# Kernel optimization log

Hardware: AMD Instinct MI355X
Metric: run time of the kernel (lower is better)

The kernel has to match this reference:

```python
import jax, jax.numpy as jnp
import numpy as np

B = 1
L_IMG, L_TMP, L_TXT = 1024, 1024, 256
D, H, HD, MLP = 1024, 16, 64, 4096
L = L_TXT + L_IMG + L_TMP
EPS = 1e-6
ATTN_SCALE = float(1.0 / np.sqrt(HD))


def setup_inputs() -> dict:
    key = jax.random.key(0)
    ks = jax.random.split(key, 12)
    s = 0.02  # keep activations stable
    return {
        'img': jax.random.normal(ks[0], (B, L_IMG, D), jnp.float32),
        'temporal': jax.random.normal(ks[1], (B, L_TMP, D), jnp.float32),
        'txt': jax.random.normal(ks[2], (B, L_TXT, D), jnp.float32),
        'vec': jax.random.normal(ks[3], (B, D), jnp.float32),
        'pe': jax.random.normal(ks[4], (B, 1, L, HD // 2, 2, 2), jnp.float32),
        'mod_w': jax.random.normal(ks[5], (3, D, 6 * D), jnp.float32) * s,
        'mod_b': jnp.zeros((3, 6 * D), jnp.float32),
        'qkv_w': jax.random.normal(ks[6], (3, D, 3 * D), jnp.float32) * s,
        'q_scale': jnp.ones((3, HD), jnp.float32),
        'k_scale': jnp.ones((3, HD), jnp.float32),
        'proj_w': jax.random.normal(ks[7], (3, D, D), jnp.float32) * s,
        'proj_b': jnp.zeros((3, D), jnp.float32),
        'mlp_w1': jax.random.normal(ks[8], (3, D, MLP), jnp.float32) * s,
        'mlp_b1': jnp.zeros((3, MLP), jnp.float32),
        'mlp_w2': jax.random.normal(ks[9], (3, MLP, D), jnp.float32) * s,
        'mlp_b2': jnp.zeros((3, D), jnp.float32),
    }


def _ln(x):
    # LayerNorm, elementwise_affine=False, eps=1e-6
    m = jnp.mean(x, axis=-1, keepdims=True)
    v = jnp.mean((x - m) ** 2, axis=-1, keepdims=True)
    return (x - m) * jax.lax.rsqrt(v + EPS)


def _rms(x, scale):
    # flux QKNorm RMSNorm with learnable per-head-dim scale
    return x * jax.lax.rsqrt(jnp.mean(x * x, axis=-1, keepdims=True) + EPS) * scale


def _rope(x, pe):
    # x: (B,H,L,HD), pe: (B,1,L,HD//2,2,2)
    xr = x.reshape(*x.shape[:-1], -1, 1, 2)
    out = pe[..., 0] * xr[..., 0] + pe[..., 1] * xr[..., 1]  # (B,H,L,HD//2,2)
    return out.reshape(x.shape)


def _forward(img, temporal, txt, vec, pe, mod_w, mod_b, qkv_w, q_scale, k_scale,
             proj_w, proj_b, mlp_w1, mlp_b1, mlp_w2, mlp_b2):
    sv = jax.nn.silu(vec)  # (B,D)

    def mods(i):
        m = (sv @ mod_w[i] + mod_b[i])[:, None, :]  # (B,1,6D)
        return jnp.split(m, 6, axis=-1)  # shift1, scale1, gate1, shift2, scale2, gate2

    def qkv_stream(x, i, shift1, scale1):
        xm = (1.0 + scale1) * _ln(x) + shift1
        qkv = (xm @ qkv_w[i]).reshape(x.shape[0], x.shape[1], 3, H, HD)
        q, k, v = jnp.moveaxis(qkv, 2, 0)  # each (B,Ls,H,HD)
        q = jnp.swapaxes(q, 1, 2)
        k = jnp.swapaxes(k, 1, 2)
        v = jnp.swapaxes(v, 1, 2)  # (B,H,Ls,HD)
        return _rms(q, q_scale[i]), _rms(k, k_scale[i]), v

    i_sh1, i_sc1, i_g1, i_sh2, i_sc2, i_g2 = mods(0)
    t_sh1, t_sc1, t_g1, t_sh2, t_sc2, t_g2 = mods(1)
    x_sh1, x_sc1, x_g1, x_sh2, x_sc2, x_g2 = mods(2)

    img_q, img_k, img_v = qkv_stream(img, 0, i_sh1, i_sc1)
    tmp_q, tmp_k, tmp_v = qkv_stream(temporal, 1, t_sh1, t_sc1)
    txt_q, txt_k, txt_v = qkv_stream(txt, 2, x_sh1, x_sc1)

    q = jnp.concatenate((txt_q, img_q, tmp_q), axis=2)
    k = jnp.concatenate((txt_k, img_k, tmp_k), axis=2)
    # NOTE: faithful to source bug: v concat uses temporal_q, not temporal_v
    v = jnp.concatenate((txt_v, img_v, tmp_q), axis=2)

    q = _rope(q, pe)
    k = _rope(k, pe)
    scores = jnp.einsum('bhqd,bhkd->bhqk', q, k) * ATTN_SCALE
    attn = jnp.einsum('bhqk,bhkd->bhqd', jax.nn.softmax(scores, axis=-1), v)
    attn = jnp.swapaxes(attn, 1, 2).reshape(attn.shape[0], L, H * HD)  # (B,L,D)

    txt_a = attn[:, :L_TXT]
    img_a = attn[:, L_TXT:L_TXT + L_IMG]
    tmp_a = attn[:, L_TXT + L_IMG:]

    def mlp(x, i):
        return jax.nn.gelu(x @ mlp_w1[i] + mlp_b1[i], approximate=True) @ mlp_w2[i] + mlp_b2[i]

    img = img + i_g1 * (img_a @ proj_w[0] + proj_b[0])
    img = img + i_g2 * mlp((1.0 + i_sc2) * _ln(img) + i_sh2, 0)
    temporal = temporal + t_g1 * (tmp_a @ proj_w[1] + proj_b[1])
    # NOTE: faithful to source bug: temporal_norm2 is applied to (updated) img
    temporal = temporal + t_g2 * mlp((1.0 + t_sc2) * _ln(img) + t_sh2, 1)
    txt = txt + x_g1 * (txt_a @ proj_w[2] + proj_b[2])
    txt = txt + x_g2 * mlp((1.0 + x_sc2) * _ln(txt) + x_sh2, 2)
    return img, temporal, txt


def reference(img, temporal, txt, vec, pe, mod_w, mod_b, qkv_w, q_scale, k_scale,
              proj_w, proj_b, mlp_w1, mlp_b1, mlp_w2, mlp_b2):
    return _forward(img, temporal, txt, vec, pe, mod_w, mod_b, qkv_w, q_scale,
                    k_scale, proj_w, proj_b, mlp_w1, mlp_b1, mlp_w2, mlp_b2)
```

## Files before the change

### kernel.cpp

```cpp
#include <hip/hip_runtime.h>
#include <hip/hip_bf16.h>

#define L_TXT 256
#define L_IMG 1024
#define L_TMP 1024
#define LTOT  2304
#define DMODEL 1024
#define NH 16
#define HDIM 64
#define DMLP 4096
#define EPSV 1e-6f

typedef unsigned short ushort;
typedef __attribute__((ext_vector_type(8))) short short8b;
typedef __attribute__((ext_vector_type(8))) unsigned short ushort8v;
typedef __attribute__((ext_vector_type(4))) float f32x4;
typedef __attribute__((ext_vector_type(4))) unsigned short ushort4v;

#define MOD_OFF    ((size_t)0)
#define XM_OFF     ((size_t)73728)
#define QKV_OFF    ((size_t)4792320)
#define QB_OFF     ((size_t)18948096)
#define KB_OFF     ((size_t)23666688)
#define VTB_OFF    ((size_t)28385280)
#define ATT_OFF    ((size_t)33103872)
#define S1_OFF     ((size_t)37822464)
#define QKVWT_OFF  ((size_t)49356800)
#define PROJWT_OFF ((size_t)68231168)
#define W1T_OFF    ((size_t)74522624)
#define W2T_OFF    ((size_t)99688448)
#define W2T_END    ((size_t)124854272)

static __device__ __forceinline__ ushort f2bf(float x) {
    __hip_bfloat16 b = __float2bfloat16(x);
    return *reinterpret_cast<ushort*>(&b);
}
static __device__ __forceinline__ float bf2f(ushort u) {
    return __uint_as_float(((unsigned)u) << 16);
}

typedef __attribute__((address_space(1))) const unsigned char gas_t;
typedef __attribute__((address_space(3))) unsigned char las_t;
static __device__ __forceinline__ void gload16(const void* g, void* l) {
    __builtin_amdgcn_global_load_lds((gas_t*)g, (las_t*)l, 16, 0, 0);
}

__global__ __launch_bounds__(256) void k_conv(const float* __restrict__ vec,
                                              const float* __restrict__ modw,
                                              float* __restrict__ modp,
                                              const float* __restrict__ qkvw,
                                              const float* __restrict__ projw,
                                              const float* __restrict__ w1,
                                              const float* __restrict__ w2,
                                              ushort* __restrict__ qkvwt,
                                              ushort* __restrict__ projwt,
                                              ushort* __restrict__ w1t,
                                              ushort* __restrict__ w2t) {
    __shared__ float tb[64][132];
    int bid = blockIdx.x;
    int tid = threadIdx.x;
    if (bid < 576) {
        float* svs = &tb[0][0];
        float* pl  = &tb[0][0] + 256;
        int g0 = (bid >> 2) * 128;
        int ks = bid & 3;
        int i  = g0 / 6144;
        int j0 = g0 - i * 6144;
        {
            float v = vec[ks*256 + tid];
            svs[tid] = v / (1.0f + __expf(-v));
        }
        __syncthreads();
        int jl = tid & 31, ko = tid >> 5;
        const float* wp = modw + (size_t)i * 1024 * 6144 + (size_t)(ks*256) * 6144 + j0 + jl*4;
        float a0x=0.f,a0y=0.f,a0z=0.f,a0w=0.f;
        float a1x=0.f,a1y=0.f,a1z=0.f,a1w=0.f;
#pragma unroll 4
        for (int kk = 0; kk < 16; kk++) {
            int k0 = kk*16 + ko;
            int k1 = k0 + 8;
            float4 w0 = *reinterpret_cast<const float4*>(wp + (size_t)k0 * 6144);
            float4 w1v = *reinterpret_cast<const float4*>(wp + (size_t)k1 * 6144);
            float s0 = svs[k0], s1 = svs[k1];
            a0x += s0*w0.x; a0y += s0*w0.y; a0z += s0*w0.z; a0w += s0*w0.w;
            a1x += s1*w1v.x; a1y += s1*w1v.y; a1z += s1*w1v.z; a1w += s1*w1v.w;
        }
        pl[ko*128 + jl*4+0] = a0x + a1x;
        pl[ko*128 + jl*4+1] = a0y + a1y;
        pl[ko*128 + jl*4+2] = a0z + a1z;
        pl[ko*128 + jl*4+3] = a0w + a1w;
        __syncthreads();
        if (tid < 128) {
            float s = 0.f;
#pragma unroll
            for (int k = 0; k < 8; k++) s += pl[k*128 + tid];
            modp[(size_t)ks*18432 + g0 + tid] = s;
        }
        return;
    }
    int b = bid - 576;
    const float* W; ushort* WT; int K, N, nt, kt;
    if (b < 1152) {
        int s = b / 384, r = b % 384;
        K = 1024; N = 3072; nt = r % 24; kt = r / 24;
        W = qkvw + (size_t)s * K * N; WT = qkvwt + (size_t)s * N * K;
    } else if (b < 1536) {
        b -= 1152; int s = b / 128, r = b % 128;
        K = 1024; N = 1024; nt = r % 8; kt = r / 8;
        W = projw + (size_t)s * K * N; WT = projwt + (size_t)s * N * K;
    } else if (b < 3072) {
        b -= 1536; int s = b / 512, r = b % 512;
        K = 1024; N = 4096; nt = r % 32; kt = r / 32;
        W = w1 + (size_t)s * K * N; WT = w1t + (size_t)s * N * K;
    } else {
        b -= 3072; int s = b / 512, r = b % 512;
        K = 4096; N = 1024; nt = r % 8; kt = r / 8;
        W = w2 + (size_t)s * K * N; WT = w2t + (size_t)s * N * K;
    }
    {
        int r = tid >> 5, c4 = (tid & 31) * 4;
#pragma unroll
        for (int i = 0; i < 8; i++) {
            float4 v = *reinterpret_cast<const float4*>(W + (size_t)(kt*64 + r + i*8) * N + nt*128 + c4);
            tb[r + i*8][c4+0] = v.x; tb[r + i*8][c4+1] = v.y;
            tb[r + i*8][c4+2] = v.z; tb[r + i*8][c4+3] = v.w;
        }
    }
    __syncthreads();
    {
        int n = tid >> 1, k32 = (tid & 1) * 32;
        ushort* dst = WT + (size_t)(nt*128 + n) * K + kt*64 + k32;
#pragma unroll
        for (int j2 = 0; j2 < 4; j2++) {
            ushort8v u;
#pragma unroll
            for (int i = 0; i < 8; i++) u[i] = f2bf(tb[k32 + j2*8 + i][n]);
            *reinterpret_cast<ushort8v*>(dst + j2*8) = u;
        }
    }
}

__global__ __launch_bounds__(256) void k_modr(const float* __restrict__ p,
                                              const float* __restrict__ modb,
                                              float* __restrict__ mod) {
    int g = blockIdx.x * 256 + threadIdx.x;
    float s = p[g] + p[18432 + g] + p[2*18432 + g] + p[3*18432 + g];
    mod[g] = s + modb[g];
}

__global__ __launch_bounds__(256) void k_conv_slice(const float* __restrict__ W,
                                                    ushort* __restrict__ WT,
                                                    int K, int N) {
    __shared__ float tb[64][132];
    int nt = blockIdx.x, kt = blockIdx.y, tid = threadIdx.x;
    {
        int r = tid >> 5, c4 = (tid & 31) * 4;
#pragma unroll
        for (int i = 0; i < 8; i++) {
            float4 v = *reinterpret_cast<const float4*>(W + (size_t)(kt*64 + r + i*8) * N + nt*128 + c4);
            tb[r + i*8][c4+0] = v.x; tb[r + i*8][c4+1] = v.y;
            tb[r + i*8][c4+2] = v.z; tb[r + i*8][c4+3] = v.w;
        }
    }
    __syncthreads();
    {
        int n = tid >> 1, k32 = (tid & 1) * 32;
        ushort* dst = WT + (size_t)(nt*128 + n) * K + kt*64 + k32;
#pragma unroll
        for (int j2 = 0; j2 < 4; j2++) {
            ushort8v u;
#pragma unroll
            for (int i = 0; i < 8; i++) u[i] = f2bf(tb[k32 + j2*8 + i][n]);
            *reinterpret_cast<ushort8v*>(dst + j2*8) = u;
        }
    }
}

__global__ __launch_bounds__(256) void k_ln_mod1(const float* __restrict__ img,
                                                 const float* __restrict__ tmp,
                                                 const float* __restrict__ txt,
                                                 const float* __restrict__ mod,
                                                 ushort* __restrict__ xm) {
    int l = blockIdx.x;
    const float* src; int strm;
    if (l < L_TXT)              { src = txt + (size_t)l * DMODEL;            strm = 2; }
    else if (l < L_TXT + L_IMG) { src = img + (size_t)(l - L_TXT) * DMODEL;  strm = 0; }
    else                        { src = tmp + (size_t)(l - L_TXT - L_IMG) * DMODEL; strm = 1; }

    int d = threadIdx.x * 4;
    float4 x = *reinterpret_cast<const float4*>(src + d);
    float s  = x.x + x.y + x.z + x.w;
    float s2 = x.x*x.x + x.y*x.y + x.z*x.z + x.w*x.w;
#pragma unroll
    for (int o = 32; o > 0; o >>= 1) { s += __shfl_xor(s, o); s2 += __shfl_xor(s2, o); }
    __shared__ float red[8];
    int wave = threadIdx.x >> 6, lane = threadIdx.x & 63;
    if (lane == 0) { red[wave*2] = s; red[wave*2+1] = s2; }
    __syncthreads();
    if (threadIdx.x == 0) {
        float a = 0.f, b = 0.f;
        for (int w = 0; w < 4; w++) { a += red[w*2]; b += red[w*2+1]; }
        red[0] = a; red[1] = b;
    }
    __syncthreads();
    float mean = red[0] * (1.0f/DMODEL);
    float var  = red[1] * (1.0f/DMODEL) - mean*mean;
    float inv  = rsqrtf(var + EPSV);

    const float* sh = mod + strm*6144;
    const float* sc = sh + 1024;
    float4 shv = *reinterpret_cast<const float4*>(sh + d);
    float4 scv = *reinterpret_cast<const float4*>(sc + d);
    ushort4v o;
    o.x = f2bf((1.f+scv.x)*((x.x-mean)*inv) + shv.x);
    o.y = f2bf((1.f+scv.y)*((x.y-mean)*inv) + shv.y);
    o.z = f2bf((1.f+scv.z)*((x.z-mean)*inv) + shv.z);
    o.w = f2bf((1.f+scv.w)*((x.w-mean)*inv) + shv.w);
    *reinterpret_cast<ushort4v*>(xm + (size_t)l*DMODEL + d) = o;
}

__global__ __launch_bounds__(256) void k_ln_mod2(const float* __restrict__ src,
                                                 const float* __restrict__ sh,
                                                 const float* __restrict__ sc,
                                                 ushort* __restrict__ out) {
    int r = blockIdx.x;
    const float* srow = src + (size_t)r * DMODEL;
    int d = threadIdx.x * 4;
    float4 x = *reinterpret_cast<const float4*>(srow + d);
    float s  = x.x + x.y + x.z + x.w;
    float s2 = x.x*x.x + x.y*x.y + x.z*x.z + x.w*x.w;
#pragma unroll
    for (int o = 32; o > 0; o >>= 1) { s += __shfl_xor(s, o); s2 += __shfl_xor(s2, o); }
    __shared__ float red[8];
    int wave = threadIdx.x >> 6, lane = threadIdx.x & 63;
    if (lane == 0) { red[wave*2] = s; red[wave*2+1] = s2; }
    __syncthreads();
    if (threadIdx.x == 0) {
        float a = 0.f, b = 0.f;
        for (int w = 0; w < 4; w++) { a += red[w*2]; b += red[w*2+1]; }
        red[0] = a; red[1] = b;
    }
    __syncthreads();
    float mean = red[0] * (1.0f/DMODEL);
    float var  = red[1] * (1.0f/DMODEL) - mean*mean;
    float inv  = rsqrtf(var + EPSV);
    float4 shv = *reinterpret_cast<const float4*>(sh + d);
    float4 scv = *reinterpret_cast<const float4*>(sc + d);
    ushort4v o;
    o.x = f2bf((1.f+scv.x)*((x.x-mean)*inv) + shv.x);
    o.y = f2bf((1.f+scv.y)*((x.y-mean)*inv) + shv.y);
    o.z = f2bf((1.f+scv.z)*((x.z-mean)*inv) + shv.z);
    o.w = f2bf((1.f+scv.w)*((x.w-mean)*inv) + shv.w);
    *reinterpret_cast<ushort4v*>(out + (size_t)r*DMODEL + d) = o;
}

__global__ __launch_bounds__(256) void k_ln_modg(const float* __restrict__ s1,
                                                 const float* __restrict__ mod,
                                                 ushort* __restrict__ xm) {
    int row = blockIdx.x;
    int strm = row < 256 ? 2 : 0;
    const float* srow = s1 + (size_t)row * DMODEL;
    int d = threadIdx.x * 4;
    float4 x = *reinterpret_cast<const float4*>(srow + d);
    float s  = x.x + x.y + x.z + x.w;
    float s2 = x.x*x.x + x.y*x.y + x.z*x.z + x.w*x.w;
#pragma unroll
    for (int o = 32; o > 0; o >>= 1) { s += __shfl_xor(s, o); s2 += __shfl_xor(s2, o); }
    __shared__ float red[8];
    int wave = threadIdx.x >> 6, lane = threadIdx.x & 63;
    if (lane == 0) { red[wave*2] = s; red[wave*2+1] = s2; }
    __syncthreads();
    if (threadIdx.x == 0) {
        float a = 0.f, b = 0.f;
        for (int w = 0; w < 4; w++) { a += red[w*2]; b += red[w*2+1]; }
        red[0] = a; red[1] = b;
    }
    __syncthreads();
    float mean = red[0] * (1.0f/DMODEL);
    float var  = red[1] * (1.0f/DMODEL) - mean*mean;
    float inv  = rsqrtf(var + EPSV);
    const float* sh = mod + strm*6144 + 3*1024;
    const float* sc = mod + strm*6144 + 4*1024;
    float4 shv = *reinterpret_cast<const float4*>(sh + d);
    float4 scv = *reinterpret_cast<const float4*>(sc + d);
    ushort4v o;
    o.x = f2bf((1.f+scv.x)*((x.x-mean)*inv) + shv.x);
    o.y = f2bf((1.f+scv.y)*((x.y-mean)*inv) + shv.y);
    o.z = f2bf((1.f+scv.z)*((x.z-mean)*inv) + shv.z);
    o.w = f2bf((1.f+scv.w)*((x.w-mean)*inv) + shv.w);
    *reinterpret_cast<ushort4v*>(xm + (size_t)row*DMODEL + d) = o;
}

__device__ __forceinline__ float gelu_fast(float x) {
    return x / (1.0f + __expf(-1.5957691216057308f * (x + 0.044715f * x * x * x)));
}

template<int MODE, int BM, int BN, typename OutT>
__global__ __launch_bounds__(256) void k_gemm_ms(const ushort* __restrict__ A_t,
                                                 const ushort* __restrict__ A_i,
                                                 const ushort* __restrict__ A_m,
                                                 const ushort* __restrict__ BT,
                                                 const float* __restrict__ bias,
                                                 const float* __restrict__ res_t,
                                                 const float* __restrict__ res_i,
                                                 const float* __restrict__ res_m,
                                                 const float* __restrict__ mod, int gidx,
                                                 OutT* __restrict__ out_t,
                                                 OutT* __restrict__ out_i,
                                                 OutT* __restrict__ out_m,
                                                 int N, int K, int ry0) {
    constexpr int MI = BM / 32;
    constexpr int NI = BN / 32;
    const int brow = (ry0 + blockIdx.y) * BM;
    int s, lrow;
    if (brow < 256)       { s = 2; lrow = brow; }
    else if (brow < 1280) { s = 0; lrow = brow - 256; }
    else                  { s = 1; lrow = brow - 1280; }

    const ushort* A = (s==2 ? A_t : s==0 ? A_i : A_m) + (size_t)lrow * K;
    const ushort* BTs = BT + (size_t)s * N * K;
    const float* bi = (MODE != 3 && bias) ? bias + (size_t)s * N : nullptr;
    const float* resl = (MODE==2) ? ((s==2 ? res_t : s==0 ? res_i : res_m) + (size_t)lrow * N) : nullptr;
    const float* gate = (MODE==2) ? (mod + s*6144 + gidx*1024) : nullptr;
    OutT* Cl;
    if (MODE == 3) Cl = (blockIdx.z == 0 ? out_t : out_i) + (size_t)brow * N;
    else           Cl = (s==2 ? out_t : s==0 ? out_i : out_m) + (size_t)lrow * N;

    const int kbeg = (MODE == 3) ? blockIdx.z * (K >> 1) : 0;
    const int kend = (MODE == 3) ? kbeg + (K >> 1) : K;

    __shared__ ushort Asl[BM*64];
    __shared__ ushort Bsl[BN*64];
    const int tid = threadIdx.x;
    const int lane = tid & 63, w = tid >> 6;
    const int wr = w >> 1, wc = w & 1;
    const int bn = blockIdx.x * BN;
    const int r15 = lane & 15, g4 = lane >> 4;

    f32x4 acc[MI][NI];
#pragma unroll
    for (int i = 0; i < MI; i++)
#pragma unroll
        for (int j = 0; j < NI; j++) acc[i][j] = (f32x4){0.f,0.f,0.f,0.f};

    for (int k0 = kbeg; k0 < kend; k0 += 64) {
#pragma unroll
        for (int i = 0; i < BM/32; i++) {
            int chunk = i*4 + w;
            int seg = chunk*64 + lane;
            int row = seg >> 3;
            int gs  = (seg & 7) ^ (row & 7);
            gload16(A + (size_t)row * K + k0 + gs*8, Asl + (size_t)chunk * 512);
        }
#pragma unroll
        for (int i = 0; i < BN/32; i++) {
            int chunk = i*4 + w;
            int seg = chunk*64 + lane;
            int row = seg >> 3;
            int gs  = (seg & 7) ^ (row & 7);
            gload16(BTs + (size_t)(bn + row) * K + k0 + gs*8, Bsl + (size_t)chunk * 512);
        }
        __syncthreads();
#pragma unroll
        for (int kk = 0; kk < 2; kk++) {
            short8b a[MI], b[NI];
#pragma unroll
            for (int mi = 0; mi < MI; mi++) {
                int row = wr*(MI*16) + mi*16 + r15;
                int c   = kk*4 + g4;
                a[mi] = *reinterpret_cast<const short8b*>(&Asl[row*64 + ((c ^ (row & 7)))*8]);
            }
#pragma unroll
            for (int ni = 0; ni < NI; ni++) {
                int row = wc*(NI*16) + ni*16 + r15;
                int c   = kk*4 + g4;
                b[ni] = *reinterpret_cast<const short8b*>(&Bsl[row*64 + ((c ^ (row & 7)))*8]);
            }
#pragma unroll
            for (int mi = 0; mi < MI; mi++)
#pragma unroll
                for (int ni = 0; ni < NI; ni++)
                    acc[mi][ni] = __builtin_amdgcn_mfma_f32_16x16x32_bf16(a[mi], b[ni], acc[mi][ni], 0, 0, 0);
        }
        __syncthreads();
    }

#pragma unroll
    for (int mi = 0; mi < MI; mi++) {
#pragma unroll
        for (int ni = 0; ni < NI; ni++) {
            int col = bn + wc*(NI*16) + ni*16 + r15;
            float bv = bi ? bi[col] : 0.f;
#pragma unroll
            for (int r = 0; r < 4; r++) {
                int rr = wr*(MI*16) + mi*16 + g4*4 + r;
                float v = acc[mi][ni][r] + bv;
                if (MODE == 1) v = gelu_fast(v);
                if (MODE == 2) v = resl[(size_t)rr * N + col] + gate[col] * v;
                if (sizeof(OutT) == 2) Cl[(size_t)rr * N + col] = (OutT)f2bf(v);
                else                   Cl[(size_t)rr * N + col] = (OutT)v;
            }
        }
    }
}

__global__ __launch_bounds__(256) void k_mlp2fin(const float* __restrict__ p0,
                                                 const float* __restrict__ p1,
                                                 const float* __restrict__ b2,
                                                 const float* __restrict__ s1,
                                                 const float* __restrict__ mod,
                                                 float* __restrict__ out_t,
                                                 float* __restrict__ out_i,
                                                 float* __restrict__ out_m,
                                                 int row0) {
    int row = row0 + blockIdx.x;
    int s, lrow;
    if (row < 256)       { s = 2; lrow = row; }
    else if (row < 1280) { s = 0; lrow = row - 256; }
    else                 { s = 1; lrow = row - 1280; }
    const float* gate = mod + s*6144 + 5*1024;
    const float* bias = b2 + s*1024;
    float* outp = (s==2 ? out_t : s==0 ? out_i : out_m) + (size_t)lrow * DMODEL;
    int d = threadIdx.x * 4;
    float4 a = *reinterpret_cast<const float4*>(p0 + (size_t)row*DMODEL + d);
    float4 b = *reinterpret_cast<const float4*>(p1 + (size_t)row*DMODEL + d);
    float4 r = *reinterpret_cast<const float4*>(s1 + (size_t)row*DMODEL + d);
    float4 g = *reinterpret_cast<const float4*>(gate + d);
    float4 bi = *reinterpret_cast<const float4*>(bias + d);
    float4 o;
    o.x = r.x + g.x*(a.x + b.x + bi.x);
    o.y = r.y + g.y*(a.y + b.y + bi.y);
    o.z = r.z + g.z*(a.z + b.z + bi.z);
    o.w = r.w + g.w*(a.w + b.w + bi.w);
    *reinterpret_cast<float4*>(outp + d) = o;
}

__global__ __launch_bounds__(256) void k_qkvfin(const ushort* __restrict__ qkv,
                                                const float* __restrict__ pe,
                                                const float* __restrict__ qs,
                                                const float* __restrict__ ks,
                                                ushort* __restrict__ Q,
                                                ushort* __restrict__ K,
                                                ushort* __restrict__ VT) {
    const int tid = threadIdx.x;
    const int w = tid >> 6, lane = tid & 63;
    const int h  = blockIdx.x / 36;
    const int l0 = (blockIdx.x % 36) * 64;
    __shared__ ushort vbuf[64][65];

    for (int it = 0; it < 16; it++) {
        int ll = it*4 + w;
        int l = l0 + ll;
        int strm;
        if (l < L_TXT) strm = 2; else if (l < L_TXT + L_IMG) strm = 0; else strm = 1;
        const ushort* row = qkv + (size_t)l * 3 * DMODEL + h*HDIM + lane;
        float q = bf2f(row[0]);
        float k = bf2f(row[DMODEL]);
        float v = bf2f(row[2*DMODEL]);

        float sq = q*q, sk = k*k;
#pragma unroll
        for (int o = 32; o > 0; o >>= 1) { sq += __shfl_xor(sq, o); sk += __shfl_xor(sk, o); }
        float rq = q * rsqrtf(sq * (1.0f/HDIM) + EPSV) * qs[strm*HDIM + lane];
        float rk = k * rsqrtf(sk * (1.0f/HDIM) + EPSV) * ks[strm*HDIM + lane];

        float vout = (strm == 1) ? rq : v;

        float rq_p = __shfl_xor(rq, 1);
        float rk_p = __shfl_xor(rk, 1);
        float qe = (lane & 1) ? rq_p : rq;
        float qo = (lane & 1) ? rq : rq_p;
        float ke = (lane & 1) ? rk_p : rk;
        float ko = (lane & 1) ? rk : rk_p;
        const float* pel = pe + (size_t)l*128 + (lane >> 1)*4 + (lane & 1)*2;
        float qr = pel[0]*qe + pel[1]*qo;
        float kr = pel[0]*ke + pel[1]*ko;

        size_t idx = ((size_t)h * LTOT + l) * HDIM + lane;
        Q[idx] = f2bf(qr);
        K[idx] = f2bf(kr);
        vbuf[ll][lane] = f2bf(vout);
    }
    __syncthreads();
    {
        int d = tid >> 2, ls = (tid & 3) * 16;
        ushort8v u0, u1;
#pragma unroll
        for (int i = 0; i < 8; i++) u0[i] = vbuf[ls+i][d];
#pragma unroll
        for (int i = 0; i < 8; i++) u1[i] = vbuf[ls+8+i][d];
        ushort* dst = VT + ((size_t)h * 64 + d) * LTOT + l0 + ls;
        *reinterpret_cast<ushort8v*>(dst)     = u0;
        *reinterpret_cast<ushort8v*>(dst + 8) = u1;
    }
}

__global__ __launch_bounds__(256) void k_attn_mfma(const ushort* __restrict__ Qb,
                                                   const ushort* __restrict__ Kb,
                                                   const ushort* __restrict__ VTb,
                                                   ushort* __restrict__ att) {
    const int tid = threadIdx.x;
    const int w = tid >> 6, lane = tid & 63;
    const int h  = blockIdx.x / 36;
    const int qt = blockIdx.x % 36;
    const int qbase = qt*64 + w*16;
    const int g = lane >> 4;
    const int q = lane & 15;

    __shared__ ushort Ksl[2][64*64];
    __shared__ ushort Vsl[2][64*64];
    __shared__ ushort plds[4][1024];
    ushort* P = plds[w];

    const ushort* Kg = Kb  + (size_t)h * LTOT * 64;
    const ushort* Vg = VTb + (size_t)h * 64 * LTOT;

    const ushort* qp = Qb + ((size_t)h * LTOT + qbase + q) * 64 + g*8;
    const short8b qf0 = *reinterpret_cast<const short8b*>(qp);
    const short8b qf1 = *reinterpret_cast<const short8b*>(qp + 32);

    f32x4 out[4];
#pragma unroll
    for (int d = 0; d < 4; d++) out[d] = (f32x4){0.f,0.f,0.f,0.f};
    float m = -1e30f, lsum = 0.f;

#pragma unroll
    for (int i = 0; i < 2; i++) {
        int seg = i*256 + tid;
        int row = seg >> 3;
        int gs  = (seg & 7) ^ (row & 7);
        gload16(Kg + (size_t)row*64 + gs*8, &Ksl[0][(size_t)(i*256 + w*64)*8]);
        gload16(Vg + (size_t)row*LTOT + gs*8, &Vsl[0][(size_t)(i*256 + w*64)*8]);
    }

    for (int t = 0; t < 36; t++) {
        const int cb = t & 1;
        __syncthreads();
        if (t < 35) {
            int kvn = (t+1) * 64;
#pragma unroll
            for (int i = 0; i < 2; i++) {
                int seg = i*256 + tid;
                int row = seg >> 3;
                int gs  = (seg & 7) ^ (row & 7);
                gload16(Kg + (size_t)(kvn + row)*64 + gs*8, &Ksl[cb^1][(size_t)(i*256 + w*64)*8]);
                gload16(Vg + (size_t)row*LTOT + kvn + gs*8, &Vsl[cb^1][(size_t)(i*256 + w*64)*8]);
            }
        }

        f32x4 s[4];
        __builtin_amdgcn_s_setprio(1);
#pragma unroll
        for (int ks = 0; ks < 4; ks++) {
            int r = ks*16 + q;
            short8b kf0 = *reinterpret_cast<const short8b*>(&Ksl[cb][r*64 + ((g     ^ (r & 7)))*8]);
            short8b kf1 = *reinterpret_cast<const short8b*>(&Ksl[cb][r*64 + (((4+g) ^ (r & 7)))*8]);
            f32x4 acc = (f32x4){0.f,0.f,0.f,0.f};
            acc = __builtin_amdgcn_mfma_f32_16x16x32_bf16(kf0, qf0, acc, 0, 0, 0);
            acc = __builtin_amdgcn_mfma_f32_16x16x32_bf16(kf1, qf1, acc, 0, 0, 0);
            s[ks] = acc;
        }
        __builtin_amdgcn_s_setprio(0);

        float m0 = fmaxf(fmaxf(s[0][0], s[0][1]), s[0][2]);
        float m1 = fmaxf(fmaxf(s[0][3], s[1][0]), s[1][1]);
        float m2 = fmaxf(fmaxf(s[1][2], s[1][3]), s[2][0]);
        float m3 = fmaxf(fmaxf(s[2][1], s[2][2]), s[2][3]);
        float m4 = fmaxf(fmaxf(s[3][0], s[3][1]), s[3][2]);
        float t5 = fmaxf(fmaxf(m0, m1), m2);
        float t6 = fmaxf(fmaxf(m3, m4), s[3][3]);
        float tmax = fmaxf(t5, t6);
        tmax = fmaxf(tmax, __shfl_xor(tmax, 16));
        tmax = fmaxf(tmax, __shfl_xor(tmax, 32));
        float pm = tmax * 0.125f;
        if (!__all(pm <= m)) {
            float newm = fmaxf(m, pm);
            float c = __expf(m - newm);
            lsum *= c;
#pragma unroll
            for (int d = 0; d < 4; d++) out[d] *= c;
            m = newm;
        }
        float p[16];
        float tsum = 0.f;
#pragma unroll
        for (int ks = 0; ks < 4; ks++)
#pragma unroll
            for (int r = 0; r < 4; r++) {
                float pv = __expf(s[ks][r] * 0.125f - m);
                p[ks*4+r] = pv;
                tsum += pv;
            }
        tsum += __shfl_xor(tsum, 16);
        tsum += __shfl_xor(tsum, 32);
        lsum += tsum;

#pragma unroll
        for (int ks = 0; ks < 4; ks++) {
            ushort4v pk;
            pk.x = f2bf(p[ks*4+0]); pk.y = f2bf(p[ks*4+1]);
            pk.z = f2bf(p[ks*4+2]); pk.w = f2bf(p[ks*4+3]);
            int widx = (q*64 + ks*16 + g*4) ^ ((q & 7) << 3);
            *reinterpret_cast<ushort4v*>(&P[widx]) = pk;
        }
        __builtin_amdgcn_s_setprio(1);
#pragma unroll
        for (int c2 = 0; c2 < 2; c2++) {
            int ridx = (q*64 + c2*32 + g*8) ^ ((q & 7) << 3);
            short8b pf = *reinterpret_cast<const short8b*>(&P[ridx]);
#pragma unroll
            for (int ds = 0; ds < 4; ds++) {
                int d = ds*16 + q;
                short8b vf = *reinterpret_cast<const short8b*>(&Vsl[cb][d*64 + (((c2*4+g) ^ (d & 7)))*8]);
                out[ds] = __builtin_amdgcn_mfma_f32_16x16x32_bf16(vf, pf, out[ds], 0, 0, 0);
            }
        }
        __builtin_amdgcn_s_setprio(0);
    }

    float inv = 1.0f / lsum;
    ushort* orow = att + (size_t)(qbase + q) * DMODEL + h * HDIM;
#pragma unroll
    for (int ds = 0; ds < 4; ds++) {
        ushort4v o4;
        o4.x = f2bf(out[ds][0]*inv); o4.y = f2bf(out[ds][1]*inv);
        o4.z = f2bf(out[ds][2]*inv); o4.w = f2bf(out[ds][3]*inv);
        *reinterpret_cast<ushort4v*>(orow + ds*16 + g*4) = o4;
    }
}

extern "C" void kernel_launch(void* const* d_in, const int* in_sizes, int n_in,
                              void* d_out, int out_size, void* d_ws, size_t ws_size,
                              hipStream_t stream) {
    const float* img  = (const float*)d_in[0];
    const float* tmp  = (const float*)d_in[1];
    const float* txt  = (const float*)d_in[2];
    const float* vec  = (const float*)d_in[3];
    const float* pe   = (const float*)d_in[4];
    const float* modw = (const float*)d_in[5];
    const float* modb = (const float*)d_in[6];
    const float* qkvw = (const float*)d_in[7];
    const float* qsc  = (const float*)d_in[8];
    const float* ksc  = (const float*)d_in[9];
    const float* projw= (const float*)d_in[10];
    const float* projb= (const float*)d_in[11];
    const float* w1   = (const float*)d_in[12];
    const float* b1   = (const float*)d_in[13];
    const float* w2   = (const float*)d_in[14];
    const float* b2   = (const float*)d_in[15];

    char* wsb = (char*)d_ws;
    float*  mod    = (float*) (wsb + MOD_OFF);
    ushort* xm     = (ushort*)(wsb + XM_OFF);
    ushort* qkv    = (ushort*)(wsb + QKV_OFF);
    ushort* t1     = (ushort*)(wsb + QKV_OFF);
    ushort* Qb     = (ushort*)(wsb + QB_OFF);
    ushort* Kb     = (ushort*)(wsb + KB_OFF);
    ushort* VTb    = (ushort*)(wsb + VTB_OFF);
    float*  p0buf  = (float*) (wsb + QB_OFF);
    float*  p1buf  = (float*) (wsb + VTB_OFF);
    float*  modp   = (float*) (wsb + ATT_OFF);
    ushort* att    = (ushort*)(wsb + ATT_OFF);
    float*  s1     = (float*) (wsb + S1_OFF);
    ushort* qkvwt  = (ushort*)(wsb + QKVWT_OFF);
    ushort* projwt = (ushort*)(wsb + PROJWT_OFF);
    ushort* w1t    = (ushort*)(wsb + W1T_OFF);

    const bool bigws = ws_size >= W2T_END;
    ushort* w2t = bigws ? (ushort*)(wsb + W2T_OFF) : w1t;

    float* out_img = (float*)d_out;
    float* out_tmp = out_img + (size_t)L_IMG * DMODEL;
    float* out_txt = out_tmp + (size_t)L_TMP * DMODEL;

    int conv_blocks = 576 + (bigws ? 4608 : 3072);
    k_conv<<<conv_blocks, 256, 0, stream>>>(vec, modw, modp,
                                            qkvw, projw, w1, w2,
                                            qkvwt, projwt, w1t, w2t);
    k_modr<<<72, 256, 0, stream>>>(modp, modb, mod);
    k_ln_mod1<<<LTOT, 256, 0, stream>>>(img, tmp, txt, mod, xm);

    k_gemm_ms<0, 128, 128, ushort><<<dim3(24, 18), 256, 0, stream>>>(
        xm, xm + (size_t)256*DMODEL, xm + (size_t)1280*DMODEL,
        qkvwt, nullptr, nullptr, nullptr, nullptr, nullptr, 0,
        qkv, qkv + (size_t)256*3072, qkv + (size_t)1280*3072, 3072, DMODEL, 0);

    k_qkvfin<<<NH*36, 256, 0, stream>>>(qkv, pe, qsc, ksc, Qb, Kb, VTb);
    k_attn_mfma<<<NH*36, 256, 0, stream>>>(Qb, Kb, VTb, att);

    k_gemm_ms<2, 64, 128, float><<<dim3(8, 36), 256, 0, stream>>>(
        att, att + (size_t)256*DMODEL, att + (size_t)1280*DMODEL,
        projwt, projb, txt, img, tmp, mod, 2,
        s1, s1 + (size_t)256*DMODEL, s1 + (size_t)1280*DMODEL, DMODEL, DMODEL, 0);

    k_ln_modg<<<1280, 256, 0, stream>>>(s1, mod, xm);
    k_gemm_ms<1, 128, 128, ushort><<<dim3(32, 10), 256, 0, stream>>>(
        xm, xm + (size_t)256*DMODEL, xm + (size_t)1280*DMODEL,
        w1t, b1, nullptr, nullptr, nullptr, nullptr, 0,
        t1, t1 + (size_t)256*DMLP, t1, DMLP, DMODEL, 0);
    if (!bigws) {
        k_conv_slice<<<dim3(8, 64), 256, 0, stream>>>(w2,                          w1t,                          DMLP, DMODEL);
        k_conv_slice<<<dim3(8, 64), 256, 0, stream>>>(w2 + (size_t)2*DMLP*DMODEL,  w1t + (size_t)2*DMLP*DMODEL,  DMLP, DMODEL);
    }
    k_gemm_ms<3, 64, 128, float><<<dim3(8, 20, 2), 256, 0, stream>>>(
        t1, t1 + (size_t)256*DMLP, t1,
        w2t, nullptr, nullptr, nullptr, nullptr, nullptr, 0,
        p0buf, p1buf, nullptr, DMODEL, DMLP, 0);
    k_mlp2fin<<<1280, 256, 0, stream>>>(p0buf, p1buf, b2, s1, mod,
                                        out_txt, out_img, out_tmp, 0);

    k_ln_mod2<<<L_TMP, 256, 0, stream>>>(out_img, mod + 1*6144 + 3*1024, mod + 1*6144 + 4*1024, xm + (size_t)1280*DMODEL);
    k_gemm_ms<1, 128, 128, ushort><<<dim3(32, 8), 256, 0, stream>>>(
        xm, xm + (size_t)256*DMODEL, xm + (size_t)1280*DMODEL,
        w1t, b1, nullptr, nullptr, nullptr, nullptr, 0,
        t1, t1, t1, DMLP, DMODEL, 10);
    if (!bigws) {
        k_conv_slice<<<dim3(8, 64), 256, 0, stream>>>(w2 + (size_t)DMLP*DMODEL, w1t + (size_t)DMLP*DMODEL, DMLP, DMODEL);
    }
    k_gemm_ms<3, 64, 128, float><<<dim3(8, 16, 2), 256, 0, stream>>>(
        t1, t1, t1,
        w2t, nullptr, nullptr, nullptr, nullptr, nullptr, 0,
        p0buf, p1buf, nullptr, DMODEL, DMLP, 20);
    k_mlp2fin<<<1024, 256, 0, stream>>>(p0buf, p1buf, b2, s1, mod,
                                        out_txt, out_img, out_tmp, 1280);
}
```

Baseline: 316.6 us.

## Overlap weight conversion with QKV GEMM and shrink MLP1 GEMM tiles

Splits the monolithic weight-conversion kernel so only the mod and QKV weight conversion runs first. The proj, w1 and w2 transposes now run as extra blocks inside a new fused QKV GEMM kernel, so that conversion can overlap with the QKV matmul. Those transposes use nontemporal loads and stores to avoid polluting the cache. The MLP1 GEMMs also switch to 64-row tiles with twice as many blocks for better occupancy, at the cost of less tile reuse. The risk is that the GEMM blocks now compete with memory-bound conversion blocks for bandwidth and LDS.

```diff
diff --git a/kernel.cpp b/kernel.cpp
--- a/kernel.cpp
+++ b/kernel.cpp
@@ -45,17 +45,41 @@
     __builtin_amdgcn_global_load_lds((gas_t*)g, (las_t*)l, 16, 0, 0);
 }
 
-__global__ __launch_bounds__(256) void k_conv(const float* __restrict__ vec,
-                                              const float* __restrict__ modw,
-                                              float* __restrict__ modp,
-                                              const float* __restrict__ qkvw,
-                                              const float* __restrict__ projw,
-                                              const float* __restrict__ w1,
-                                              const float* __restrict__ w2,
-                                              ushort* __restrict__ qkvwt,
-                                              ushort* __restrict__ projwt,
-                                              ushort* __restrict__ w1t,
-                                              ushort* __restrict__ w2t) {
+template<bool NT>
+static __device__ __forceinline__ void conv_tile(const float* __restrict__ W,
+                                                 ushort* __restrict__ WT,
+                                                 int K, int N, int nt, int kt,
+                                                 float (*tb)[132], int tid) {
+    {
+        int r = tid >> 5, c4 = (tid & 31) * 4;
+#pragma unroll
+        for (int i = 0; i < 8; i++) {
+            const f32x4* src = reinterpret_cast<const f32x4*>(W + (size_t)(kt*64 + r + i*8) * N + nt*128 + c4);
+            f32x4 v = NT ? __builtin_nontemporal_load(src) : *src;
+            tb[r + i*8][c4+0] = v.x; tb[r + i*8][c4+1] = v.y;
+            tb[r + i*8][c4+2] = v.z; tb[r + i*8][c4+3] = v.w;
+        }
+    }
+    __syncthreads();
+    {
+        int n = tid >> 1, k32 = (tid & 1) * 32;
+        ushort* dst = WT + (size_t)(nt*128 + n) * K + kt*64 + k32;
+#pragma unroll
+        for (int j2 = 0; j2 < 4; j2++) {
+            ushort8v u;
+#pragma unroll
+            for (int i = 0; i < 8; i++) u[i] = f2bf(tb[k32 + j2*8 + i][n]);
+            if (NT) __builtin_nontemporal_store(u, reinterpret_cast<ushort8v*>(dst + j2*8));
+            else    *reinterpret_cast<ushort8v*>(dst + j2*8) = u;
+        }
+    }
+}
+
+__global__ __launch_bounds__(256) void k_conv_a(const float* __restrict__ vec,
+                                                const float* __restrict__ modw,
+                                                float* __restrict__ modp,
+                                                const float* __restrict__ qkvw,
+                                                ushort* __restrict__ qkvwt) {
     __shared__ float tb[64][132];
     int bid = blockIdx.x;
     int tid = threadIdx.x;
@@ -99,45 +123,9 @@
         return;
     }
     int b = bid - 576;
-    const float* W; ushort* WT; int K, N, nt, kt;
-    if (b < 1152) {
-        int s = b / 384, r = b % 384;
-        K = 1024; N = 3072; nt = r % 24; kt = r / 24;
-        W = qkvw + (size_t)s * K * N; WT = qkvwt + (size_t)s * N * K;
-    } else if (b < 1536) {
-        b -= 1152; int s = b / 128, r = b % 128;
-        K = 1024; N = 1024; nt = r % 8; kt = r / 8;
-        W = projw + (size_t)s * K * N; WT = projwt + (size_t)s * N * K;
-    } else if (b < 3072) {
-        b -= 1536; int s = b / 512, r = b % 512;
-        K = 1024; N = 4096; nt = r % 32; kt = r / 32;
-        W = w1 + (size_t)s * K * N; WT = w1t + (size_t)s * N * K;
-    } else {
-        b -= 3072; int s = b / 512, r = b % 512;
-        K = 4096; N = 1024; nt = r % 8; kt = r / 8;
-        W = w2 + (size_t)s * K * N; WT = w2t + (size_t)s * N * K;
-    }
-    {
-        int r = tid >> 5, c4 = (tid & 31) * 4;
-#pragma unroll
-        for (int i = 0; i < 8; i++) {
-            float4 v = *reinterpret_cast<const float4*>(W + (size_t)(kt*64 + r + i*8) * N + nt*128 + c4);
-            tb[r + i*8][c4+0] = v.x; tb[r + i*8][c4+1] = v.y;
-            tb[r + i*8][c4+2] = v.z; tb[r + i*8][c4+3] = v.w;
-        }
-    }
-    __syncthreads();
-    {
-        int n = tid >> 1, k32 = (tid & 1) * 32;
-        ushort* dst = WT + (size_t)(nt*128 + n) * K + kt*64 + k32;
-#pragma unroll
-        for (int j2 = 0; j2 < 4; j2++) {
-            ushort8v u;
-#pragma unroll
-            for (int i = 0; i < 8; i++) u[i] = f2bf(tb[k32 + j2*8 + i][n]);
-            *reinterpret_cast<ushort8v*>(dst + j2*8) = u;
-        }
-    }
+    int s = b / 384, r = b % 384;
+    conv_tile<false>(qkvw + (size_t)s * 1024 * 3072, qkvwt + (size_t)s * 3072 * 1024,
+                     1024, 3072, r % 24, r / 24, tb, tid);
 }
 
 __global__ __launch_bounds__(256) void k_modr(const float* __restrict__ p,
@@ -152,26 +140,117 @@
                                                     ushort* __restrict__ WT,
                                                     int K, int N) {
     __shared__ float tb[64][132];
-    int nt = blockIdx.x, kt = blockIdx.y, tid = threadIdx.x;
-    {
-        int r = tid >> 5, c4 = (tid & 31) * 4;
-#pragma unroll
-        for (int i = 0; i < 8; i++) {
-            float4 v = *reinterpret_cast<const float4*>(W + (size_t)(kt*64 + r + i*8) * N + nt*128 + c4);
-            tb[r + i*8][c4+0] = v.x; tb[r + i*8][c4+1] = v.y;
-            tb[r + i*8][c4+2] = v.z; tb[r + i*8][c4+3] = v.w;
-        }
-    }
-    __syncthreads();
-    {
-        int n = tid >> 1, k32 = (tid & 1) * 32;
-        ushort* dst = WT + (size_t)(nt*128 + n) * K + kt*64 + k32;
-#pragma unroll
-        for (int j2 = 0; j2 < 4; j2++) {
-            ushort8v u;
-#pragma unroll
-            for (int i = 0; i < 8; i++) u[i] = f2bf(tb[k32 + j2*8 + i][n]);
-            *reinterpret_cast<ushort8v*>(dst + j2*8) = u;
+    conv_tile<false>(W, WT, K, N, blockIdx.x, blockIdx.y, tb, threadIdx.x);
+}
+
+__global__ __launch_bounds__(256) void k_qkv_conv(const ushort* __restrict__ xm,
+                                                  const ushort* __restrict__ qkvwt,
+                                                  ushort* __restrict__ qkv,
+                                                  const float* __restrict__ projw,
+                                                  const float* __restrict__ w1,
+                                                  const float* __restrict__ w2,
+                                                  ushort* __restrict__ projwt,
+                                                  ushort* __restrict__ w1t,
+                                                  ushort* __restrict__ w2t) {
+    __shared__ union {
+        struct { ushort A[128*64]; ushort B[128*64]; } g;
+        float tb[64][132];
+    } sm;
+    const int tid = threadIdx.x;
+
+    if (blockIdx.x >= 432) {
+        int b = blockIdx.x - 432;
+        if (b < 384) {
+            int s = b / 128, r = b % 128;
+            conv_tile<true>(projw + (size_t)s * 1024 * 1024, projwt + (size_t)s * 1024 * 1024,
+                            1024, 1024, r % 8, r / 8, sm.tb, tid);
+        } else if (b < 1920) {
+            b -= 384; int s = b / 512, r = b % 512;
+            conv_tile<true>(w1 + (size_t)s * 1024 * 4096, w1t + (size_t)s * 4096 * 1024,
+                            1024, 4096, r % 32, r / 32, sm.tb, tid);
+        } else {
+            b -= 1920; int s = b / 512, r = b % 512;
+            conv_tile<true>(w2 + (size_t)s * 4096 * 1024, w2t + (size_t)s * 1024 * 4096,
+                            4096, 1024, r % 8, r / 8, sm.tb, tid);
+        }
+        return;
+    }
+
+    const int nx = blockIdx.x % 24, ny = blockIdx.x / 24;
+    const int brow = ny * 128;
+    int s;
+    if (brow < 256)       { s = 2; }
+    else if (brow < 1280) { s = 0; }
+    else                  { s = 1; }
+    const int arow = brow;
+
+    const ushort* A = xm + (size_t)arow * DMODEL;
+    const ushort* BTs = qkvwt + (size_t)s * 3072 * 1024;
+    ushort* Cl = qkv + (size_t)arow * 3072;
+
+    const int lane = tid & 63, w = tid >> 6;
+    const int wr = w >> 1, wc = w & 1;
+    const int bn = nx * 128;
+    const int r15 = lane & 15, g4 = lane >> 4;
+
+    f32x4 acc[4][4];
+#pragma unroll
+    for (int i = 0; i < 4; i++)
+#pragma unroll
+        for (int j = 0; j < 4; j++) acc[i][j] = (f32x4){0.f,0.f,0.f,0.f};
+
+    for (int k0 = 0; k0 < 1024; k0 += 64) {
+#pragma unroll
+        for (int i = 0; i < 4; i++) {
+            int chunk = i*4 + w;
+            int seg = chunk*64 + lane;
+            int row = seg >> 3;
+            int gs  = (seg & 7) ^ (row & 7);
+            gload16(A + (size_t)row * 1024 + k0 + gs*8, sm.g.A + (size_t)chunk * 512);
+        }
+#pragma unroll
+        for (int i = 0; i < 4; i++) {
+            int chunk = i*4 + w;
+            int seg = chunk*64 + lane;
+            int row = seg >> 3;
+            int gs  = (seg & 7) ^ (row & 7);
+            gload16(BTs + (size_t)(bn + row) * 1024 + k0 + gs*8, sm.g.B + (size_t)chunk * 512);
+        }
+        __syncthreads();
+#pragma unroll
+        for (int kk = 0; kk < 2; kk++) {
+            short8b a[4], b[4];
+#pragma unroll
+            for (int mi = 0; mi < 4; mi++) {
+                int row = wr*64 + mi*16 + r15;
+                int c   = kk*4 + g4;
+                a[mi] = *reinterpret_cast<const short8b*>(&sm.g.A[row*64 + ((c ^ (row & 7)))*8]);
+            }
+#pragma unroll
+            for (int ni = 0; ni < 4; ni++) {
+                int row = wc*64 + ni*16 + r15;
+                int c   = kk*4 + g4;
+                b[ni] = *reinterpret_cast<const short8b*>(&sm.g.B[row*64 + ((c ^ (row & 7)))*8]);
+            }
+#pragma unroll
+            for (int mi = 0; mi < 4; mi++)
+#pragma unroll
+                for (int ni = 0; ni < 4; ni++)
+                    acc[mi][ni] = __builtin_amdgcn_mfma_f32_16x16x32_bf16(a[mi], b[ni], acc[mi][ni], 0, 0, 0);
+        }
+        __syncthreads();
+    }
+
+#pragma unroll
+    for (int mi = 0; mi < 4; mi++) {
+#pragma unroll
+        for (int ni = 0; ni < 4; ni++) {
+            int col = bn + wc*64 + ni*16 + r15;
+#pragma unroll
+            for (int r = 0; r < 4; r++) {
+                int rr = wr*64 + mi*16 + g4*4 + r;
+                Cl[(size_t)rr * 3072 + col] = f2bf(acc[mi][ni][r]);
+            }
         }
     }
 }
@@ -673,17 +752,13 @@
     float* out_tmp = out_img + (size_t)L_IMG * DMODEL;
     float* out_txt = out_tmp + (size_t)L_TMP * DMODEL;
 
-    int conv_blocks = 576 + (bigws ? 4608 : 3072);
-    k_conv<<<conv_blocks, 256, 0, stream>>>(vec, modw, modp,
-                                            qkvw, projw, w1, w2,
-                                            qkvwt, projwt, w1t, w2t);
+    k_conv_a<<<576 + 1152, 256, 0, stream>>>(vec, modw, modp, qkvw, qkvwt);
     k_modr<<<72, 256, 0, stream>>>(modp, modb, mod);
     k_ln_mod1<<<LTOT, 256, 0, stream>>>(img, tmp, txt, mod, xm);
 
-    k_gemm_ms<0, 128, 128, ushort><<<dim3(24, 18), 256, 0, stream>>>(
-        xm, xm + (size_t)256*DMODEL, xm + (size_t)1280*DMODEL,
-        qkvwt, nullptr, nullptr, nullptr, nullptr, nullptr, 0,
-        qkv, qkv + (size_t)256*3072, qkv + (size_t)1280*3072, 3072, DMODEL, 0);
+    int qc_blocks = 432 + (bigws ? 3456 : 1920);
+    k_qkv_conv<<<qc_blocks, 256, 0, stream>>>(xm, qkvwt, qkv,
+                                              projw, w1, w2, projwt, w1t, w2t);
 
     k_qkvfin<<<NH*36, 256, 0, stream>>>(qkv, pe, qsc, ksc, Qb, Kb, VTb);
     k_attn_mfma<<<NH*36, 256, 0, stream>>>(Qb, Kb, VTb, att);
@@ -694,7 +769,7 @@
         s1, s1 + (size_t)256*DMODEL, s1 + (size_t)1280*DMODEL, DMODEL, DMODEL, 0);
 
     k_ln_modg<<<1280, 256, 0, stream>>>(s1, mod, xm);
-    k_gemm_ms<1, 128, 128, ushort><<<dim3(32, 10), 256, 0, stream>>>(
+    k_gemm_ms<1, 64, 128, ushort><<<dim3(32, 20), 256, 0, stream>>>(
         xm, xm + (size_t)256*DMODEL, xm + (size_t)1280*DMODEL,
         w1t, b1, nullptr, nullptr, nullptr, nullptr, 0,
         t1, t1 + (size_t)256*DMLP, t1, DMLP, DMODEL, 0);
@@ -710,10 +785,10 @@
                                         out_txt, out_img, out_tmp, 0);
 
     k_ln_mod2<<<L_TMP, 256, 0, stream>>>(out_img, mod + 1*6144 + 3*1024, mod + 1*6144 + 4*1024, xm + (size_t)1280*DMODEL);
-    k_gemm_ms<1, 128, 128, ushort><<<dim3(32, 8), 256, 0, stream>>>(
+    k_gemm_ms<1, 64, 128, ushort><<<dim3(32, 16), 256, 0, stream>>>(
         xm, xm + (size_t)256*DMODEL, xm + (size_t)1280*DMODEL,
         w1t, b1, nullptr, nullptr, nullptr, nullptr, 0,
-        t1, t1, t1, DMLP, DMODEL, 10);
+        t1, t1, t1, DMLP, DMODEL, 20);
     if (!bigws) {
         k_conv_slice<<<dim3(8, 64), 256, 0, stream>>>(w2 + (size_t)DMLP*DMODEL, w1t + (size_t)DMLP*DMODEL, DMLP, DMODEL);
     }
```

Result: slower. 373.0 us (+17.8%).
